# Kernel optimization log

Measured on AMD Instinct MI355X. Metric: run time of the kernel, lower is better.

Reference implementation:

```python
import jax, jax.numpy as jnp
import numpy as np
from jax import lax

T, B, F, H = 128, 256, 512, 1024
NEG_SLOPE = 0.01  # torch LeakyReLU default


def leaky_relu(x):
    return jnp.where(x >= 0, x, NEG_SLOPE * x)


def setup_inputs() -> dict:
    key = jax.random.key(0)
    ks = jax.random.split(key, 10)
    s1 = 1.0 / np.sqrt(F)
    sh = 1.0 / np.sqrt(H)
    return {
        "x": jax.random.normal(ks[0], (T, B, F), dtype=jnp.float32),
        "dones": jax.random.randint(ks[1], (T, B), 0, 2, dtype=jnp.int32),
        "W1": jax.random.uniform(ks[2], (H, F), jnp.float32, -s1, s1),
        "b1": jax.random.uniform(ks[3], (H,), jnp.float32, -s1, s1),
        "W_ih": jax.random.uniform(ks[4], (4 * H, H), jnp.float32, -sh, sh),
        "W_hh": jax.random.uniform(ks[5], (4 * H, H), jnp.float32, -sh, sh),
        "b_ih": jax.random.uniform(ks[6], (4 * H,), jnp.float32, -sh, sh),
        "b_hh": jax.random.uniform(ks[7], (4 * H,), jnp.float32, -sh, sh),
        "Wv": jax.random.uniform(ks[8], (1, H), jnp.float32, -sh, sh),
        "bv": jax.random.uniform(ks[9], (1,), jnp.float32, -sh, sh),
    }


def _forward(x, dones, W1, b1, W_ih, W_hh, b_ih, b_hh, Wv, bv):
    # shared_net: Linear + LeakyReLU, applied to all timesteps at once
    shared = leaky_relu(jnp.einsum("tbf,hf->tbh", x, W1) + b1)  # [T,B,H]
    # precompute input contribution to all gates (i,f,g,o order as in torch)
    x_gates = jnp.einsum("tbh,gh->tbg", shared, W_ih) + b_ih + b_hh  # [T,B,4H]
    reset = (dones == 0).astype(x.dtype)[:, :, None]  # [T,B,1], 0 where done

    def step(carry, inp):
        h, c = carry  # [B,H] each
        xg, m = inp
        # mask-reset hidden state where episode ended, then detach (torch .detach())
        h = lax.stop_gradient(h * m)
        c = lax.stop_gradient(c * m)
        gates = xg + h @ W_hh.T  # [B,4H]
        i, f, g, o = jnp.split(gates, 4, axis=-1)
        i = jax.nn.sigmoid(i)
        f = jax.nn.sigmoid(f)
        g = jnp.tanh(g)
        o = jax.nn.sigmoid(o)
        c = f * c + i * g
        h = o * jnp.tanh(c)
        return (h, c), h

    h0 = jnp.zeros((x.shape[1], W_hh.shape[1]), x.dtype)
    (hT, cT), hs = lax.scan(step, (h0, h0), (x_gates, reset))
    value = leaky_relu(hs) @ Wv.T + bv  # [T,B,1]
    hidden = jnp.stack([hT, cT], axis=0)  # [2*num_layers, B, H]
    return value, hidden


def reference(x, dones, W1, b1, W_ih, W_hh, b_ih, b_hh, Wv, bv):
    return _forward(x, dones, W1, b1, W_ih, W_hh, b_ih, b_hh, Wv, bv)
```

## Files before the change

kernel.cpp:

```cpp
#include <hip/hip_runtime.h>
#include <cstdint>
#include <cstddef>

#define T_DIM 128
#define B_DIM 256
#define F_DIM 512
#define H_DIM 1024
#define G_DIM 4096

typedef unsigned short u16;
typedef unsigned short u16x8 __attribute__((ext_vector_type(8)));
typedef unsigned short u16x4 __attribute__((ext_vector_type(4)));
typedef __bf16 bf16x8 __attribute__((ext_vector_type(8)));
typedef float f32x4 __attribute__((ext_vector_type(4)));
typedef unsigned long long u64;

__device__ __forceinline__ float bf2f(u16 u) {
    union { unsigned v; float f; } x; x.v = ((unsigned)u) << 16; return x.f;
}
__device__ __forceinline__ u16 f2bf(float f) {
    union { float f; unsigned v; } x; x.f = f;
    return (u16)((x.v + 0x7fffu + ((x.v >> 16) & 1u)) >> 16);
}

__device__ __forceinline__ f32x4 mfma16(u16x8 a, u16x8 b, f32x4 c) {
    return __builtin_amdgcn_mfma_f32_16x16x32_bf16(
        __builtin_bit_cast(bf16x8, a), __builtin_bit_cast(bf16x8, b), c, 0, 0, 0);
}

template <int AUX>
__device__ __forceinline__ void gl_lds16(const void* g, void* s) {
    __builtin_amdgcn_global_load_lds(
        (const __attribute__((address_space(1))) void*)g,
        (__attribute__((address_space(3))) void*)s, 16, 0, AUX);
}

__device__ __forceinline__ float sigm(float x) { return 1.0f / (1.0f + __expf(-x)); }
__device__ __forceinline__ float tanh_fast(float x) {
    float e = __expf(2.0f * x);
    return 1.0f - 2.0f / (e + 1.0f);
}

template <int EPI>
__global__ __launch_bounds__(256) void gemm_bt128(
    const u16* __restrict__ A, const u16* __restrict__ B,
    const float* __restrict__ bias, u16* __restrict__ C, int K, int N) {
    __shared__ __align__(16) u16 smem[128 * 136];
    u16* lA = smem;
    u16* lB = smem + 8192;
    const int lane = threadIdx.x & 63;
    const int wave = threadIdx.x >> 6;
    const int wr = wave >> 1, wc = wave & 1;
    const int bm = blockIdx.x, bn = blockIdx.y;
    f32x4 acc[4][4] = {};
    const int srow = lane >> 3;
    const int scol = (lane & 7) * 8;
    const u16* Abase = A + (size_t)(bm * 128 + srow) * K + scol;
    const u16* Bbase = B + (size_t)(bn * 128 + srow) * K + scol;

    for (int k0 = 0; k0 < K; k0 += 64) {
#pragma unroll
        for (int j = 0; j < 4; ++j) {
            int chunk = wave * 4 + j;
            gl_lds16<0>(Abase + (size_t)(chunk * 8) * K + k0, lA + chunk * 512);
            gl_lds16<0>(Bbase + (size_t)(chunk * 8) * K + k0, lB + chunk * 512);
        }
        __syncthreads();
        const u16* pA = lA + (wr * 64 + (lane & 15)) * 64 + (lane >> 4) * 8;
        const u16* pB = lB + (wc * 64 + (lane & 15)) * 64 + (lane >> 4) * 8;
#pragma unroll
        for (int kk = 0; kk < 2; ++kk) {
            u16x8 a[4], b[4];
#pragma unroll
            for (int m = 0; m < 4; ++m) a[m] = *(const u16x8*)(pA + m * 1024 + kk * 32);
#pragma unroll
            for (int n = 0; n < 4; ++n) b[n] = *(const u16x8*)(pB + n * 1024 + kk * 32);
#pragma unroll
            for (int m = 0; m < 4; ++m)
#pragma unroll
                for (int n = 0; n < 4; ++n)
                    acc[m][n] = mfma16(a[m], b[n], acc[m][n]);
        }
        __syncthreads();
    }
#pragma unroll
    for (int n = 0; n < 4; ++n) {
        int cc = wc * 64 + n * 16 + (lane & 15);
        float bv = bias[bn * 128 + cc];
#pragma unroll
        for (int m = 0; m < 4; ++m) {
            int rr = wr * 64 + m * 16 + ((lane >> 4) * 4);
#pragma unroll
            for (int i = 0; i < 4; ++i) {
                float v = acc[m][n][i] + bv;
                if (EPI == 1) v = (v >= 0.0f) ? v : 0.01f * v;
                smem[(rr + i) * 136 + cc] = f2bf(v);
            }
        }
    }
    __syncthreads();
#pragma unroll
    for (int p = 0; p < 8; ++p) {
        int rr = p * 16 + wave * 4 + (lane >> 4);
        int cc = (lane & 15) * 8;
        u16x8 v = *(const u16x8*)(smem + rr * 136 + cc);
        *(u16x8*)(C + (size_t)(bm * 128 + rr) * N + bn * 128 + cc) = v;
    }
}


__device__ __forceinline__ void stage_chunk_blk(const char* hinB, int bm, char* buf,
                                                int kc, int wave, int lane) {
#pragma unroll
    for (int j = 0; j < 8; ++j) {
        int hr = wave * 8 + j;
        int r = hr * 2 + (lane >> 5);
        int sc = ((lane & 31) * 16) ^ ((r & 7) << 4);
        int cbg = kc * 512 + sc;
        gl_lds16<17>(hinB + (size_t)(cbg >> 5) * 8192 + bm * 2048 + r * 32 + (cbg & 31),
                     buf + (size_t)hr * 1024);
    }
}

__global__ __launch_bounds__(256, 1) void lstm_seq(
    const u16* __restrict__ xg, const u16* __restrict__ Whh,
    const int* __restrict__ dones, const float* __restrict__ Wv,
    u16* __restrict__ h0, u16* __restrict__ h1,
    float* __restrict__ cbuf, float* __restrict__ hbuf,
    float* __restrict__ value, int* __restrict__ flags,
    float* __restrict__ vpartial, int t0, int nt, int first) {
    __shared__ __align__(16) char sm[65536];
    float* lepi = (float*)sm;
    char* hbB = sm + 17408;
    float* vpB = (float*)(sm + 19456);
    const int tid = threadIdx.x;
    const int lane = tid & 63, wave = tid >> 6;
    const int bm = blockIdx.x & 3, bn = blockIdx.x >> 2;
    const int sw = (lane & 7) << 4;

    u16x8 breg[32];
    {
        const u16* wrow = Whh + (size_t)(bn * 64 + wave * 16 + (lane & 15)) * H_DIM +
                          (lane >> 4) * 8;
#pragma unroll
        for (int s = 0; s < 32; ++s) breg[s] = *(const u16x8*)(wrow + s * 32);
    }

    const int r = tid & 63;
    const int ublk = tid >> 6;
    const int bg = bm * 64 + r;
    const int ucol = bn * 16 + ublk * 4;
    float wv[4], c[4];
#pragma unroll
    for (int uu = 0; uu < 4; ++uu) wv[uu] = Wv[ucol + uu];
    if (first) {
        c[0] = c[1] = c[2] = c[3] = 0.0f;
    } else {
        float4 cv = *(const float4*)(cbuf + (size_t)bg * H_DIM + ucol);
        c[0] = cv.x; c[1] = cv.y; c[2] = cv.z; c[3] = cv.w;
    }

    const int rl = lane & 15;
    const int ko = (lane >> 4) * 16;

    for (int tt = 0; tt < nt; ++tt) {
        const int t = t0 + tt;
        const char* hinB = (const char*)((t & 1) ? h1 : h0);
        u16* houtB = (t & 1) ? h0 : h1;

        auto poll16 = [&](int kc) {
            if (t > 0) {
                const int fi = bm * 64 + kc * 16 + (lane & 15);
                while (__hip_atomic_load(&flags[fi], __ATOMIC_RELAXED,
                                         __HIP_MEMORY_SCOPE_AGENT) < t)
                    __builtin_amdgcn_s_sleep(1);
            }
        };

        const int done = dones[t * B_DIM + bg];
        u16x4 xv[4];
#pragma unroll
        for (int uu = 0; uu < 4; ++uu)
            xv[uu] = *(const u16x4*)(xg + (size_t)tt * B_DIM * G_DIM +
                                     (size_t)bg * G_DIM + bn * 64 + (ublk * 4 + uu) * 4);

        poll16(0);
        stage_chunk_blk(hinB, bm, sm, 0, wave, lane);
        poll16(1);
        __syncthreads();

        f32x4 acc[4] = {};
#pragma unroll
        for (int kc = 0; kc < 4; ++kc) {
            char* buf = sm + (kc & 1) * 32768;
            if (kc < 3) stage_chunk_blk(hinB, bm, sm + ((kc + 1) & 1) * 32768, kc + 1,
                                        wave, lane);
#pragma unroll
            for (int s2 = 0; s2 < 8; ++s2) {
                int kb2 = s2 * 64 + ko;
#pragma unroll
                for (int m = 0; m < 4; ++m) {
                    u16x8 a = *(const u16x8*)(buf + (m * 16 + rl) * 512 + (kb2 ^ sw));
                    acc[m] = mfma16(a, breg[kc * 8 + s2], acc[m]);
                }
            }
            if (kc < 2) poll16(kc + 2);
            if (kc < 3) __syncthreads();
        }

#pragma unroll
        for (int m = 0; m < 4; ++m)
#pragma unroll
            for (int i = 0; i < 4; ++i)
                lepi[(m * 16 + (lane >> 4) * 4 + i) * 65 + wave * 16 + rl] = acc[m][i];

        const float mb = (done == 0) ? 1.0f : 0.0f;
        float vpart = 0.0f;
        u16x4 hb;
        float hf[4];
#pragma unroll
        for (int uu = 0; uu < 4; ++uu) {
            const float* gp = &lepi[r * 65 + (ublk * 4 + uu) * 4];
            float gi = bf2f(xv[uu][0]) + mb * gp[0];
            float gf = bf2f(xv[uu][1]) + mb * gp[1];
            float gg = bf2f(xv[uu][2]) + mb * gp[2];
            float go = bf2f(xv[uu][3]) + mb * gp[3];
            float i_ = sigm(gi), f_ = sigm(gf), g_ = tanh_fast(gg), o_ = sigm(go);
            float cn = f_ * (mb * c[uu]) + i_ * g_;
            float hn = o_ * tanh_fast(cn);
            c[uu] = cn; hf[uu] = hn;
            hb[uu] = f2bf(hn);
            float lr = (hn >= 0.0f) ? hn : 0.01f * hn;
            vpart += lr * wv[uu];
        }
        *(u16x4*)(hbB + r * 32 + ublk * 8) = hb;
        vpB[r * 4 + ublk] = vpart;
        if (t == T_DIM - 1)
            *(float4*)(hbuf + (size_t)bg * H_DIM + ucol) = make_float4(hf[0], hf[1], hf[2], hf[3]);
        __syncthreads();

        {
            u64 hv = *(const u64*)(hbB + tid * 8);
            __hip_atomic_store((u64*)((char*)houtB + (size_t)bn * 8192 + bm * 2048 + tid * 8),
                               hv, __ATOMIC_RELAXED, __HIP_MEMORY_SCOPE_AGENT);
            if (tid < 64) {
                const u64* pv = (const u64*)vpB + tid * 2;
                u64 v0 = pv[0], v1 = pv[1];
                float* dv = vpartial + (size_t)(t & 1) * 65536 + (size_t)bn * 1024 +
                            bm * 256 + tid * 4;
                __hip_atomic_store((u64*)dv, v0, __ATOMIC_RELAXED, __HIP_MEMORY_SCOPE_AGENT);
                __hip_atomic_store((u64*)dv + 1, v1, __ATOMIC_RELAXED, __HIP_MEMORY_SCOPE_AGENT);
            }
        }
        __syncthreads();
        if (tid == 0)
            __hip_atomic_store(&flags[bm * 64 + bn], t + 1, __ATOMIC_RELAXED,
                               __HIP_MEMORY_SCOPE_AGENT);

        if (t > 0 && tid < 64) {
            const float* vp = vpartial + (size_t)((t - 1) & 1) * 65536 +
                              (size_t)lane * 1024 + (size_t)(bm * 64 + bn) * 4;
            union { u64 u; float f[2]; } ua, ub;
            ua.u = __hip_atomic_load((const u64*)vp, __ATOMIC_RELAXED,
                                     __HIP_MEMORY_SCOPE_AGENT);
            ub.u = __hip_atomic_load((const u64*)(vp + 2), __ATOMIC_RELAXED,
                                     __HIP_MEMORY_SCOPE_AGENT);
            float s = ua.f[0] + ua.f[1] + ub.f[0] + ub.f[1];
#pragma unroll
            for (int m2 = 32; m2 >= 1; m2 >>= 1) s += __shfl_xor(s, m2);
            if (tid == 0) value[(t - 1) * B_DIM + bm * 64 + bn] += s;
        }
    }
    *(float4*)(cbuf + (size_t)bg * H_DIM + ucol) = make_float4(c[0], c[1], c[2], c[3]);

    if (t0 + nt == T_DIM && tid < 64) {
        while (__hip_atomic_load(&flags[bm * 64 + lane], __ATOMIC_RELAXED,
                                 __HIP_MEMORY_SCOPE_AGENT) < T_DIM)
            __builtin_amdgcn_s_sleep(1);
        const float* vp = vpartial + (size_t)((T_DIM - 1) & 1) * 65536 +
                          (size_t)lane * 1024 + (size_t)(bm * 64 + bn) * 4;
        union { u64 u; float f[2]; } ua, ub;
        ua.u = __hip_atomic_load((const u64*)vp, __ATOMIC_RELAXED, __HIP_MEMORY_SCOPE_AGENT);
        ub.u = __hip_atomic_load((const u64*)(vp + 2), __ATOMIC_RELAXED,
                                 __HIP_MEMORY_SCOPE_AGENT);
        float s = ua.f[0] + ua.f[1] + ub.f[0] + ub.f[1];
#pragma unroll
        for (int m2 = 32; m2 >= 1; m2 >>= 1) s += __shfl_xor(s, m2);
        if (tid == 0) value[(T_DIM - 1) * B_DIM + bm * 64 + bn] += s;
    }
}

__global__ void k_cast_bf16(const float* __restrict__ in, u16* __restrict__ out, int n4) {
    int i = blockIdx.x * 256 + threadIdx.x;
    if (i < n4) {
        float4 v = *(const float4*)(in + (size_t)i * 4);
        u16x4 o;
        o[0] = f2bf(v.x); o[1] = f2bf(v.y); o[2] = f2bf(v.z); o[3] = f2bf(v.w);
        *(u16x4*)(out + (size_t)i * 4) = o;
    }
}

__global__ void k_permute_w(const float* __restrict__ W, u16* __restrict__ Wp) {
    int row = blockIdx.x;
    int rin = (row & 3) * H_DIM + (row >> 2);
    int c = threadIdx.x * 4;
    float4 v = *(const float4*)(W + (size_t)rin * H_DIM + c);
    u16x4 o;
    o[0] = f2bf(v.x); o[1] = f2bf(v.y); o[2] = f2bf(v.z); o[3] = f2bf(v.w);
    *(u16x4*)(Wp + (size_t)row * H_DIM + c) = o;
}

__global__ void k_prep_bias(const float* __restrict__ b_ih, const float* __restrict__ b_hh,
                            float* __restrict__ bc) {
    int i = blockIdx.x * 256 + threadIdx.x;
    int n = i >> 2, q = i & 3;
    bc[i] = b_ih[q * H_DIM + n] + b_hh[q * H_DIM + n];
}

__global__ void k_init(float* __restrict__ value, const float* __restrict__ bv,
                       u16* __restrict__ h0, int* __restrict__ flags) {
    int i = blockIdx.x * 256 + threadIdx.x;
    if (i < B_DIM * H_DIM) h0[i] = 0;
    if (i < T_DIM * B_DIM) value[i] = *bv;
    if (i < 256) flags[i] = 0;
}

extern "C" void kernel_launch(void* const* d_in, const int* in_sizes, int n_in,
                              void* d_out, int out_size, void* d_ws, size_t ws_size,
                              hipStream_t stream) {
    const float* x     = (const float*)d_in[0];
    const int*   dones = (const int*)d_in[1];
    const float* W1    = (const float*)d_in[2];
    const float* b1    = (const float*)d_in[3];
    const float* W_ih  = (const float*)d_in[4];
    const float* W_hh  = (const float*)d_in[5];
    const float* b_ih  = (const float*)d_in[6];
    const float* b_hh  = (const float*)d_in[7];
    const float* Wv    = (const float*)d_in[8];
    const float* bv    = (const float*)d_in[9];

    float* out   = (float*)d_out;
    float* value = out;
    float* hbuf  = out + (size_t)T_DIM * B_DIM;
    float* cbuf  = hbuf + (size_t)B_DIM * H_DIM;

    const size_t per_nt = (size_t)(F_DIM + H_DIM + G_DIM) * B_DIM * 2;
    const size_t fixed = (size_t)H_DIM * F_DIM * 2 + 2 * (size_t)G_DIM * H_DIM * 2 +
                         G_DIM * 4 + 2 * (size_t)B_DIM * H_DIM * 2 +
                         2 * 65536 * 4 + 8192;
    int nt = 2;
    for (int cand = 128; cand >= 2; cand >>= 1)
        if (fixed + (size_t)cand * per_nt + 65536 <= ws_size) { nt = cand; break; }
    if (nt > T_DIM) nt = T_DIM;

    char* ws = (char*)d_ws;
    size_t off = 0;
    auto alloc = [&](size_t bytes) {
        void* p = ws + off;
        off = (off + bytes + 255) & ~(size_t)255;
        return p;
    };
    u16*   x_bf   = (u16*)alloc((size_t)nt * B_DIM * F_DIM * 2);
    u16*   shr    = (u16*)alloc((size_t)nt * B_DIM * H_DIM * 2);
    u16*   xg     = (u16*)alloc((size_t)nt * B_DIM * G_DIM * 2);
    u16*   W1b    = (u16*)alloc((size_t)H_DIM * F_DIM * 2);
    u16*   Wihp   = (u16*)alloc((size_t)G_DIM * H_DIM * 2);
    u16*   Whhp   = (u16*)alloc((size_t)G_DIM * H_DIM * 2);
    float* bcomb  = (float*)alloc((size_t)G_DIM * 4);
    u16*   hping  = (u16*)alloc((size_t)B_DIM * H_DIM * 2);
    u16*   hpong  = (u16*)alloc((size_t)B_DIM * H_DIM * 2);
    int*   flags  = (int*)alloc(256 * 4);
    float* vpart  = (float*)alloc(2 * 65536 * 4);

    k_cast_bf16<<<(H_DIM * F_DIM / 4) / 256, 256, 0, stream>>>(W1, W1b, H_DIM * F_DIM / 4);
    k_permute_w<<<G_DIM, 256, 0, stream>>>(W_ih, Wihp);
    k_permute_w<<<G_DIM, 256, 0, stream>>>(W_hh, Whhp);
    k_prep_bias<<<G_DIM / 256, 256, 0, stream>>>(b_ih, b_hh, bcomb);
    k_init<<<(B_DIM * H_DIM) / 256, 256, 0, stream>>>(value, bv, hping, flags);

    for (int t0 = 0; t0 < T_DIM; t0 += nt) {
        int m = nt * B_DIM;
        int n4 = m * F_DIM / 4;
        k_cast_bf16<<<n4 / 256, 256, 0, stream>>>(x + (size_t)t0 * B_DIM * F_DIM, x_bf, n4);
        gemm_bt128<1><<<dim3(m / 128, H_DIM / 128), 256, 0, stream>>>(
            x_bf, W1b, b1, shr, F_DIM, H_DIM);
        gemm_bt128<0><<<dim3(m / 128, G_DIM / 128), 256, 0, stream>>>(
            shr, Wihp, bcomb, xg, H_DIM, G_DIM);

        lstm_seq<<<256, 256, 0, stream>>>(
            xg, Whhp, dones, Wv, hping, hpong, cbuf, hbuf, value, flags, vpart,
            t0, nt, (t0 == 0) ? 1 : 0);
    }
}
```

Before: 1.496 ms.

## Stage all four h chunks into 128KB LDS with fine-grained vmcnt waits

Adds a templated pipelined path to the LSTM recurrence kernel. It polls all flags first, issues global-to-LDS loads for all four K chunks into 128KB of dynamic shared memory, then consumes each chunk after a partial s_waitcnt vmcnt and a barrier. This replaces the double-buffered scheme with its interleaved polls and syncthreads. It depends on the 128KB dynamic LDS attribute being accepted and on hand-counted vmcnt values matching the compiler's load ordering. If the attribute is rejected, it falls back to the old path.

After: 1.903 ms. 1.27x slower.

```diff
diff --git a/kernel.cpp b/kernel.cpp
--- a/kernel.cpp
+++ b/kernel.cpp
@@ -122,6 +122,7 @@
     }
 }
 
+template <int PIPE>
 __global__ __launch_bounds__(256, 1) void lstm_seq(
     const u16* __restrict__ xg, const u16* __restrict__ Whh,
     const int* __restrict__ dones, const float* __restrict__ Wv,
@@ -129,7 +130,7 @@
     float* __restrict__ cbuf, float* __restrict__ hbuf,
     float* __restrict__ value, int* __restrict__ flags,
     float* __restrict__ vpartial, int t0, int nt, int first) {
-    __shared__ __align__(16) char sm[65536];
+    extern __shared__ __align__(16) char sm[];
     float* lepi = (float*)sm;
     char* hbB = sm + 17408;
     float* vpB = (float*)(sm + 19456);
@@ -177,35 +178,97 @@
             }
         };
 
-        const int done = dones[t * B_DIM + bg];
+        f32x4 acc[4] = {};
+        int done;
         u16x4 xv[4];
-#pragma unroll
-        for (int uu = 0; uu < 4; ++uu)
-            xv[uu] = *(const u16x4*)(xg + (size_t)tt * B_DIM * G_DIM +
-                                     (size_t)bg * G_DIM + bn * 64 + (ublk * 4 + uu) * 4);
-
-        poll16(0);
-        stage_chunk_blk(hinB, bm, sm, 0, wave, lane);
-        poll16(1);
-        __syncthreads();
-
-        f32x4 acc[4] = {};
-#pragma unroll
-        for (int kc = 0; kc < 4; ++kc) {
-            char* buf = sm + (kc & 1) * 32768;
-            if (kc < 3) stage_chunk_blk(hinB, bm, sm + ((kc + 1) & 1) * 32768, kc + 1,
-                                        wave, lane);
+
+        if (PIPE) {
+            poll16(0); poll16(1); poll16(2); poll16(3);
+            stage_chunk_blk(hinB, bm, sm, 0, wave, lane);
+            stage_chunk_blk(hinB, bm, sm + 32768, 1, wave, lane);
+            stage_chunk_blk(hinB, bm, sm + 65536, 2, wave, lane);
+            stage_chunk_blk(hinB, bm, sm + 98304, 3, wave, lane);
+            done = dones[t * B_DIM + bg];
+#pragma unroll
+            for (int uu = 0; uu < 4; ++uu)
+                xv[uu] = *(const u16x4*)(xg + (size_t)tt * B_DIM * G_DIM +
+                                         (size_t)bg * G_DIM + bn * 64 + (ublk * 4 + uu) * 4);
+
+            asm volatile("s_waitcnt vmcnt(29)" ::: "memory");
+            __builtin_amdgcn_sched_barrier(0);
+            __builtin_amdgcn_s_barrier();
 #pragma unroll
             for (int s2 = 0; s2 < 8; ++s2) {
                 int kb2 = s2 * 64 + ko;
 #pragma unroll
                 for (int m = 0; m < 4; ++m) {
-                    u16x8 a = *(const u16x8*)(buf + (m * 16 + rl) * 512 + (kb2 ^ sw));
-                    acc[m] = mfma16(a, breg[kc * 8 + s2], acc[m]);
+                    u16x8 a = *(const u16x8*)(sm + (m * 16 + rl) * 512 + (kb2 ^ sw));
+                    acc[m] = mfma16(a, breg[s2], acc[m]);
                 }
             }
-            if (kc < 2) poll16(kc + 2);
-            if (kc < 3) __syncthreads();
+            asm volatile("s_waitcnt vmcnt(21)" ::: "memory");
+            __builtin_amdgcn_sched_barrier(0);
+            __builtin_amdgcn_s_barrier();
+#pragma unroll
+            for (int s2 = 0; s2 < 8; ++s2) {
+                int kb2 = s2 * 64 + ko;
+#pragma unroll
+                for (int m = 0; m < 4; ++m) {
+                    u16x8 a = *(const u16x8*)(sm + 32768 + (m * 16 + rl) * 512 + (kb2 ^ sw));
+                    acc[m] = mfma16(a, breg[8 + s2], acc[m]);
+                }
+            }
+            asm volatile("s_waitcnt vmcnt(13)" ::: "memory");
+            __builtin_amdgcn_sched_barrier(0);
+            __builtin_amdgcn_s_barrier();
+#pragma unroll
+            for (int s2 = 0; s2 < 8; ++s2) {
+                int kb2 = s2 * 64 + ko;
+#pragma unroll
+                for (int m = 0; m < 4; ++m) {
+                    u16x8 a = *(const u16x8*)(sm + 65536 + (m * 16 + rl) * 512 + (kb2 ^ sw));
+                    acc[m] = mfma16(a, breg[16 + s2], acc[m]);
+                }
+            }
+            asm volatile("s_waitcnt vmcnt(5)" ::: "memory");
+            __builtin_amdgcn_sched_barrier(0);
+            __builtin_amdgcn_s_barrier();
+#pragma unroll
+            for (int s2 = 0; s2 < 8; ++s2) {
+                int kb2 = s2 * 64 + ko;
+#pragma unroll
+                for (int m = 0; m < 4; ++m) {
+                    u16x8 a = *(const u16x8*)(sm + 98304 + (m * 16 + rl) * 512 + (kb2 ^ sw));
+                    acc[m] = mfma16(a, breg[24 + s2], acc[m]);
+                }
+            }
+        } else {
+            done = dones[t * B_DIM + bg];
+#pragma unroll
+            for (int uu = 0; uu < 4; ++uu)
+                xv[uu] = *(const u16x4*)(xg + (size_t)tt * B_DIM * G_DIM +
+                                         (size_t)bg * G_DIM + bn * 64 + (ublk * 4 + uu) * 4);
+            poll16(0);
+            stage_chunk_blk(hinB, bm, sm, 0, wave, lane);
+            poll16(1);
+            __syncthreads();
+#pragma unroll
+            for (int kc = 0; kc < 4; ++kc) {
+                char* buf = sm + (kc & 1) * 32768;
+                if (kc < 3) stage_chunk_blk(hinB, bm, sm + ((kc + 1) & 1) * 32768, kc + 1,
+                                            wave, lane);
+#pragma unroll
+                for (int s2 = 0; s2 < 8; ++s2) {
+                    int kb2 = s2 * 64 + ko;
+#pragma unroll
+                    for (int m = 0; m < 4; ++m) {
+                        u16x8 a = *(const u16x8*)(buf + (m * 16 + rl) * 512 + (kb2 ^ sw));
+                        acc[m] = mfma16(a, breg[kc * 8 + s2], acc[m]);
+                    }
+                }
+                if (kc < 2) poll16(kc + 2);
+                if (kc < 3) __syncthreads();
+            }
         }
 
 #pragma unroll
@@ -372,6 +435,12 @@
     int*   flags  = (int*)alloc(256 * 4);
     float* vpart  = (float*)alloc(2 * 65536 * 4);
 
+    int pipe_ok = (hipFuncSetAttribute(reinterpret_cast<const void*>(&lstm_seq<1>),
+                                       hipFuncAttributeMaxDynamicSharedMemorySize,
+                                       131072) == hipSuccess);
+    hipFuncSetAttribute(reinterpret_cast<const void*>(&lstm_seq<0>),
+                        hipFuncAttributeMaxDynamicSharedMemorySize, 65536);
+
     k_cast_bf16<<<(H_DIM * F_DIM / 4) / 256, 256, 0, stream>>>(W1, W1b, H_DIM * F_DIM / 4);
     k_permute_w<<<G_DIM, 256, 0, stream>>>(W_ih, Wihp);
     k_permute_w<<<G_DIM, 256, 0, stream>>>(W_hh, Whhp);
@@ -387,8 +456,13 @@
         gemm_bt128<0><<<dim3(m / 128, G_DIM / 128), 256, 0, stream>>>(
             shr, Wihp, bcomb, xg, H_DIM, G_DIM);
 
-        lstm_seq<<<256, 256, 0, stream>>>(
-            xg, Whhp, dones, Wv, hping, hpong, cbuf, hbuf, value, flags, vpart,
-            t0, nt, (t0 == 0) ? 1 : 0);
-    }
-}
+        if (pipe_ok)
+            lstm_seq<1><<<256, 256, 131072, stream>>>(
+                xg, Whhp, dones, Wv, hping, hpong, cbuf, hbuf, value, flags, vpart,
+                t0, nt, (t0 == 0) ? 1 : 0);
+        else
+            lstm_seq<0><<<256, 256, 65536, stream>>>(
+                xg, Whhp, dones, Wv, hping, hpong, cbuf, hbuf, value, flags, vpart,
+                t0, nt, (t0 == 0) ? 1 : 0);
+    }
+}
```
